# Performance work log

Hardware: AMD Instinct MI355X
Metric: run time of the kernel (lower is better)

## Reference

```python
import jax, jax.numpy as jnp
import numpy as np

N_NODES = 50000
N_EDGES = 600000
D_FEAT = 128
NHID = 128
N_CLASSES = 40


def gcn_conv(x, W, b, src, dst, n_nodes):
    """PyG-style GCNConv: out = D^{-1/2} (A + I) D^{-1/2} (x W) + b.

    src/dst: [E'] edge endpoints including self-loops; messages are gathered
    from src and scatter-added at dst with symmetric normalization.
    """
    h = x @ W  # [N, out] -- transform before propagate (linearity => same math)
    deg = jax.ops.segment_sum(jnp.ones_like(dst, dtype=h.dtype), dst,
                              num_segments=n_nodes)  # in-degree incl. self-loop
    dinv = jnp.where(deg > 0, jax.lax.rsqrt(deg), 0.0)
    norm = dinv[src] * dinv[dst]  # [E']
    msg = h[src] * norm[:, None]  # [E', out] gather + scale
    out = jax.ops.segment_sum(msg, dst, num_segments=n_nodes)  # scatter-add
    return out + b


def setup_inputs() -> dict:
    key = jax.random.key(0)
    ks = jax.random.split(key, 8)
    x = jax.random.normal(ks[0], (N_NODES, D_FEAT), dtype=jnp.float32)
    edge_index = jax.random.randint(ks[1], (2, N_EDGES), 0, N_NODES, dtype=jnp.int64)
    # Glorot-ish scaled params
    W1 = jax.random.normal(ks[2], (D_FEAT, NHID), dtype=jnp.float32) / np.sqrt(D_FEAT)
    b1 = jnp.zeros((NHID,), dtype=jnp.float32)
    W2 = jax.random.normal(ks[3], (NHID, NHID), dtype=jnp.float32) / np.sqrt(NHID)
    b2 = jnp.zeros((NHID,), dtype=jnp.float32)
    Wlin = jax.random.normal(ks[4], (NHID, N_CLASSES), dtype=jnp.float32) / np.sqrt(NHID)
    blin = jnp.zeros((N_CLASSES,), dtype=jnp.float32)
    return {"x": x, "edge_index": edge_index, "W1": W1, "b1": b1,
            "W2": W2, "b2": b2, "Wlin": Wlin, "blin": blin}


def reference(x, edge_index, W1, b1, W2, b2, Wlin, blin):
    n = x.shape[0]
    loop = jnp.arange(n, dtype=edge_index.dtype)
    src = jnp.concatenate([edge_index[0], loop])  # add self-loops
    dst = jnp.concatenate([edge_index[1], loop])
    h = gcn_conv(x, W1, b1, src, dst, n)
    h = jnp.tanh(h)  # dropout is identity in eval mode
    h = gcn_conv(h, W2, b2, src, dst, n)
    h = jnp.tanh(h)
    return h @ Wlin + blin  # [N, num_classes]
```

## Files before the change

### kernel.cpp

```cpp
#include <hip/hip_runtime.h>
#include <cmath>

#define D 128
#define NCLS 40
#define GG 391
#define CAP 64

typedef __bf16 bfrag __attribute__((ext_vector_type(8)));
typedef float ffrag __attribute__((ext_vector_type(4)));
typedef unsigned int u32;
typedef unsigned int u32x4 __attribute__((ext_vector_type(4)));

__device__ inline float fast_tanh(float x) {
  float ax = __builtin_fabsf(x);
  float z = __expf(-2.0f * ax);
  float r = (1.0f - z) * __builtin_amdgcn_rcpf(1.0f + z);
  return copysignf(r, x);
}

__global__ __launch_bounds__(256) void zero_deg(int* __restrict__ deg, int N) {
  int i = blockIdx.x * 256 + threadIdx.x;
  if (i < N) deg[i] = 0;
}

__global__ __launch_bounds__(256) void mega1(const float* __restrict__ A, const float* __restrict__ W1,
                                             const float* __restrict__ W2, const float* __restrict__ Wl,
                                             __bf16* __restrict__ C, int N,
                                             const int* __restrict__ src, const int* __restrict__ dst, int E,
                                             int* __restrict__ deg, int* __restrict__ csr,
                                             __bf16* __restrict__ Wt2, __bf16* __restrict__ Wlt, int EB) {
  const int b = blockIdx.x;
  const int tid = threadIdx.x;
  if (b >= GG) {
    if (b < GG + EB) {
      int e = (b - GG) * 256 + tid;
      if (e < E) {
        int s = src[e], d = dst[e];
        int pos = atomicAdd(&deg[d], 1);
        if (pos < CAP) csr[d * CAP + pos] = s;
      }
    } else {
      int j = (b - GG - EB) * 256 + tid;
      if (j < 16384) {
        Wt2[j] = (__bf16)W2[(j & 127) * D + (j >> 7)];
      } else if (j < 16384 + 48 * D) {
        int q = j - 16384;
        int n = q >> 7, k = q & 127;
        Wlt[q] = (n < NCLS) ? (__bf16)Wl[k * NCLS + n] : (__bf16)0.0f;
      }
    }
    return;
  }
  __shared__ __align__(16) __bf16 Bs[128][136];
  const int wave = tid >> 6, lane = tid & 63;
  const int row0 = b * 128 + wave * 32;
  const int koff = (lane >> 4) * 8;

  for (int i = tid; i < 128 * 128; i += 256) {
    int n = i & 127, k = i >> 7;
    Bs[n][k] = (__bf16)W1[k * D + n];
  }

  bfrag a[2][4];
#pragma unroll
  for (int mt = 0; mt < 2; ++mt) {
    int r = row0 + mt * 16 + (lane & 15);
    int rc = r < N ? r : N - 1;
    const float* p = A + (size_t)rc * D;
#pragma unroll
    for (int kk = 0; kk < 4; ++kk) {
      float4 u = *(const float4*)(p + kk * 32 + koff);
      float4 v = *(const float4*)(p + kk * 32 + koff + 4);
      bfrag f;
      f[0] = (__bf16)u.x; f[1] = (__bf16)u.y; f[2] = (__bf16)u.z; f[3] = (__bf16)u.w;
      f[4] = (__bf16)v.x; f[5] = (__bf16)v.y; f[6] = (__bf16)v.z; f[7] = (__bf16)v.w;
      a[mt][kk] = f;
    }
  }
  __syncthreads();

  ffrag acc[2][8];
#pragma unroll
  for (int mt = 0; mt < 2; ++mt)
#pragma unroll
    for (int n = 0; n < 8; ++n) acc[mt][n] = (ffrag){0.f, 0.f, 0.f, 0.f};

#pragma unroll
  for (int kk = 0; kk < 4; ++kk) {
#pragma unroll
    for (int n = 0; n < 8; ++n) {
      bfrag bb = *(const bfrag*)(&Bs[n * 16 + (lane & 15)][kk * 32 + koff]);
      acc[0][n] = __builtin_amdgcn_mfma_f32_16x16x32_bf16(a[0][kk], bb, acc[0][n], 0, 0, 0);
      acc[1][n] = __builtin_amdgcn_mfma_f32_16x16x32_bf16(a[1][kk], bb, acc[1][n], 0, 0, 0);
    }
  }

  int ocol = lane & 15;
#pragma unroll
  for (int mt = 0; mt < 2; ++mt) {
    int orow0 = row0 + mt * 16 + (lane >> 4) * 4;
#pragma unroll
    for (int n = 0; n < 8; ++n)
#pragma unroll
      for (int i = 0; i < 4; ++i) {
        int r = orow0 + i;
        if (r < N) C[(size_t)r * D + n * 16 + ocol] = (__bf16)acc[mt][n][i];
      }
  }
}

__device__ inline void gather16(const __bf16* __restrict__ t, const int* __restrict__ deg,
                                const int* __restrict__ csr, const float* __restrict__ bias,
                                __bf16 (*Hs)[136], int node0, int wave, int lane, int N) {
  const int g = lane >> 4, sl = lane & 15;
  const int nbase = node0 + wave * 4;

  int nd0 = nbase < N ? nbase : N - 1;
  int cnt0 = __builtin_amdgcn_readfirstlane(deg[nd0]);
  int jm0 = cnt0 < CAP ? cnt0 : CAP;
  int es0 = (lane < jm0) ? csr[nd0 * CAP + lane] : 0;
  int dg0 = deg[es0];
  bfrag tv0 = *(const bfrag*)(t + (size_t)nd0 * D + sl * 8);

#pragma unroll
  for (int m = 0; m < 4; ++m) {
    int cnt1 = 0, jm1 = 0, es1 = 0, dg1 = 0;
    bfrag tv1 = tv0;
    if (m < 3) {
      int nx = nbase + m + 1;
      int nd1 = nx < N ? nx : N - 1;
      cnt1 = __builtin_amdgcn_readfirstlane(deg[nd1]);
      jm1 = cnt1 < CAP ? cnt1 : CAP;
      es1 = (lane < jm1) ? csr[nd1 * CAP + lane] : 0;
      dg1 = deg[es1];
      tv1 = *(const bfrag*)(t + (size_t)nd1 * D + sl * 8);
    }

    float dv = rsqrtf((float)cnt0 + 1.0f);
    float ew = rsqrtf((float)dg0 + 1.0f) * dv;
    float selfw = (g == 0) ? dv * dv : 0.0f;
    float acc[8];
#pragma unroll
    for (int i = 0; i < 8; ++i) acc[i] = selfw * (float)tv0[i];

    for (int j = 0; j < jm0; j += 4) {
      int idx = j + g;
      int c = idx < jm0 ? idx : jm0 - 1;
      int s = __shfl(es0, c, 64);
      float wv = __shfl(ew, c, 64);
      float w = idx < jm0 ? wv : 0.0f;
      bfrag r = *(const bfrag*)(t + (size_t)s * D + sl * 8);
#pragma unroll
      for (int i = 0; i < 8; ++i) acc[i] += w * (float)r[i];
    }
#pragma unroll
    for (int i = 0; i < 8; ++i) {
      acc[i] += __shfl_xor(acc[i], 16, 64);
      acc[i] += __shfl_xor(acc[i], 32, 64);
    }

    if (g == 0) {
      float4 b0 = *(const float4*)(bias + sl * 8);
      float4 b1 = *(const float4*)(bias + sl * 8 + 4);
      bfrag o;
      o[0] = (__bf16)fast_tanh(acc[0] + b0.x);
      o[1] = (__bf16)fast_tanh(acc[1] + b0.y);
      o[2] = (__bf16)fast_tanh(acc[2] + b0.z);
      o[3] = (__bf16)fast_tanh(acc[3] + b0.w);
      o[4] = (__bf16)fast_tanh(acc[4] + b1.x);
      o[5] = (__bf16)fast_tanh(acc[5] + b1.y);
      o[6] = (__bf16)fast_tanh(acc[6] + b1.z);
      o[7] = (__bf16)fast_tanh(acc[7] + b1.w);
      *(u32x4*)&Hs[wave * 4 + m][sl * 8] = *(u32x4*)&o;
    }

    cnt0 = cnt1; jm0 = jm1; es0 = es1; dg0 = dg1; tv0 = tv1;
  }
}

__global__ __launch_bounds__(256) void gather_gemm(const __bf16* __restrict__ t, const int* __restrict__ deg,
                                                   const int* __restrict__ csr, const float* __restrict__ bias,
                                                   const __bf16* __restrict__ Wt, __bf16* __restrict__ C, int N) {
  __shared__ __align__(16) __bf16 Hs[16][136];
  const int tid = threadIdx.x;
  const int wave = tid >> 6, lane = tid & 63;
  const int g = lane >> 4, sl = lane & 15;
  const int node0 = blockIdx.x * 16;

  gather16(t, deg, csr, bias, Hs, node0, wave, lane, N);
  __syncthreads();

  const int koff = g * 8;
  bfrag a[4];
#pragma unroll
  for (int kk = 0; kk < 4; ++kk) a[kk] = *(const bfrag*)(&Hs[sl][kk * 32 + koff]);
  ffrag acc2[2];
  acc2[0] = (ffrag){0.f, 0.f, 0.f, 0.f};
  acc2[1] = (ffrag){0.f, 0.f, 0.f, 0.f};
#pragma unroll
  for (int nt = 0; nt < 2; ++nt) {
    const __bf16* wp = Wt + (size_t)(wave * 32 + nt * 16 + sl) * D;
    bfrag bfr[4];
#pragma unroll
    for (int kk = 0; kk < 4; ++kk) bfr[kk] = *(const bfrag*)(wp + kk * 32 + koff);
#pragma unroll
    for (int kk = 0; kk < 4; ++kk)
      acc2[nt] = __builtin_amdgcn_mfma_f32_16x16x32_bf16(a[kk], bfr[kk], acc2[nt], 0, 0, 0);
  }
#pragma unroll
  for (int nt = 0; nt < 2; ++nt) {
    int ccol = wave * 32 + nt * 16 + sl;
#pragma unroll
    for (int i = 0; i < 4; ++i) {
      int r = node0 + g * 4 + i;
      if (r < N) C[(size_t)r * D + ccol] = (__bf16)acc2[nt][i];
    }
  }
}

__global__ __launch_bounds__(256) void gather_head(const __bf16* __restrict__ t, const int* __restrict__ deg,
                                                   const int* __restrict__ csr, const float* __restrict__ bias,
                                                   const __bf16* __restrict__ Wlt, const float* __restrict__ blin,
                                                   float* __restrict__ out, int N) {
  __shared__ __align__(16) __bf16 Hs[16][136];
  const int tid = threadIdx.x;
  const int wave = tid >> 6, lane = tid & 63;
  const int g = lane >> 4, sl = lane & 15;
  const int node0 = blockIdx.x * 16;

  gather16(t, deg, csr, bias, Hs, node0, wave, lane, N);
  __syncthreads();

  if (wave < 3) {
    const int koff = g * 8;
    bfrag a[4];
#pragma unroll
    for (int kk = 0; kk < 4; ++kk) a[kk] = *(const bfrag*)(&Hs[sl][kk * 32 + koff]);
    ffrag acc2 = (ffrag){0.f, 0.f, 0.f, 0.f};
    const __bf16* wp = Wlt + (size_t)(wave * 16 + sl) * D;
    bfrag bfr[4];
#pragma unroll
    for (int kk = 0; kk < 4; ++kk) bfr[kk] = *(const bfrag*)(wp + kk * 32 + koff);
#pragma unroll
    for (int kk = 0; kk < 4; ++kk)
      acc2 = __builtin_amdgcn_mfma_f32_16x16x32_bf16(a[kk], bfr[kk], acc2, 0, 0, 0);

    int ccol = wave * 16 + sl;
    if (ccol < NCLS) {
      float bl = blin[ccol];
#pragma unroll
      for (int i = 0; i < 4; ++i) {
        int r = node0 + g * 4 + i;
        if (r < N) out[(size_t)r * NCLS + ccol] = acc2[i] + bl;
      }
    }
  }
}

extern "C" void kernel_launch(void* const* d_in, const int* in_sizes, int n_in,
                              void* d_out, int out_size, void* d_ws, size_t ws_size,
                              hipStream_t stream) {
  const float* x    = (const float*)d_in[0];
  const int*   ei   = (const int*)d_in[1];
  const float* W1   = (const float*)d_in[2];
  const float* b1   = (const float*)d_in[3];
  const float* W2   = (const float*)d_in[4];
  const float* b2   = (const float*)d_in[5];
  const float* Wlin = (const float*)d_in[6];
  const float* blin = (const float*)d_in[7];
  float* out = (float*)d_out;

  const int N = in_sizes[0] / D;
  const int E = in_sizes[1] / 2;
  const int* srcp = ei;
  const int* dstp = ei + E;

  char* ws = (char*)d_ws;
  int*    deg = (int*)ws;
  __bf16* Wt2 = (__bf16*)(ws + ((size_t)256 << 10));
  __bf16* Wlt = (__bf16*)(ws + ((size_t)320 << 10));
  int*    csr = (int*)(ws + ((size_t)1 << 20));
  __bf16* tb  = (__bf16*)(ws + ((size_t)16 << 20));
  __bf16* hb  = (__bf16*)(ws + ((size_t)32 << 20));

  const int nb = (N + 255) / 256;
  const int eb = (E + 255) / 256;
  const int cvb = (16384 + 48 * D + 255) / 256;
  const int gb = (N + 15) / 16;
  dim3 b256(256);

  zero_deg<<<nb, b256, 0, stream>>>(deg, N);
  mega1<<<GG + eb + cvb, b256, 0, stream>>>(x, W1, W2, Wlin, tb, N, srcp, dstp, E, deg, csr, Wt2, Wlt, eb);
  gather_gemm<<<gb, b256, 0, stream>>>(tb, deg, csr, b1, Wt2, hb, N);
  gather_head<<<gb, b256, 0, stream>>>(hb, deg, csr, b2, Wlt, blin, out, N);
}
```

Baseline: 203.4 us.

## Map one node per 16-lane group in gather instead of serial nodes per wave

The gather phase now assigns each of the four 16-lane groups in a wave its own destination node, instead of processing four nodes one after another with the neighbours split across groups. This removes the cross-group shuffle reduction and the serial per-node loop, and the four nodes' gathers proceed in parallel. Each group walks its neighbours in chunks of 16 loaded cooperatively. The wave's loop bound is now the maximum degree among its four nodes, and groups with fewer neighbours still step through the extra iterations, loading and multiplying with zero weights. The software prefetch of the next node's metadata is dropped.

```diff
diff --git a/kernel.cpp b/kernel.cpp
--- a/kernel.cpp
+++ b/kernel.cpp
@@ -113,69 +113,55 @@
                                 const int* __restrict__ csr, const float* __restrict__ bias,
                                 __bf16 (*Hs)[136], int node0, int wave, int lane, int N) {
   const int g = lane >> 4, sl = lane & 15;
-  const int nbase = node0 + wave * 4;
-
-  int nd0 = nbase < N ? nbase : N - 1;
-  int cnt0 = __builtin_amdgcn_readfirstlane(deg[nd0]);
-  int jm0 = cnt0 < CAP ? cnt0 : CAP;
-  int es0 = (lane < jm0) ? csr[nd0 * CAP + lane] : 0;
-  int dg0 = deg[es0];
-  bfrag tv0 = *(const bfrag*)(t + (size_t)nd0 * D + sl * 8);
-
-#pragma unroll
-  for (int m = 0; m < 4; ++m) {
-    int cnt1 = 0, jm1 = 0, es1 = 0, dg1 = 0;
-    bfrag tv1 = tv0;
-    if (m < 3) {
-      int nx = nbase + m + 1;
-      int nd1 = nx < N ? nx : N - 1;
-      cnt1 = __builtin_amdgcn_readfirstlane(deg[nd1]);
-      jm1 = cnt1 < CAP ? cnt1 : CAP;
-      es1 = (lane < jm1) ? csr[nd1 * CAP + lane] : 0;
-      dg1 = deg[es1];
-      tv1 = *(const bfrag*)(t + (size_t)nd1 * D + sl * 8);
-    }
-
-    float dv = rsqrtf((float)cnt0 + 1.0f);
-    float ew = rsqrtf((float)dg0 + 1.0f) * dv;
-    float selfw = (g == 0) ? dv * dv : 0.0f;
-    float acc[8];
-#pragma unroll
-    for (int i = 0; i < 8; ++i) acc[i] = selfw * (float)tv0[i];
-
-    for (int j = 0; j < jm0; j += 4) {
-      int idx = j + g;
-      int c = idx < jm0 ? idx : jm0 - 1;
-      int s = __shfl(es0, c, 64);
-      float wv = __shfl(ew, c, 64);
-      float w = idx < jm0 ? wv : 0.0f;
+  const int node = node0 + wave * 4 + g;
+  const int nd = node < N ? node : N - 1;
+  const int cnt = deg[nd];
+  const int jm = cnt < CAP ? cnt : CAP;
+  const float dv = rsqrtf((float)cnt + 1.0f);
+
+  int mx = jm;
+  int o1 = __shfl_xor(mx, 16, 64);
+  mx = mx > o1 ? mx : o1;
+  int o2 = __shfl_xor(mx, 32, 64);
+  mx = mx > o2 ? mx : o2;
+  const int jmw = __builtin_amdgcn_readfirstlane(mx);
+
+  bfrag tv = *(const bfrag*)(t + (size_t)nd * D + sl * 8);
+  const float selfw = dv * dv;
+  float acc[8];
+#pragma unroll
+  for (int i = 0; i < 8; ++i) acc[i] = selfw * (float)tv[i];
+
+  for (int base = 0; base < jmw; base += 16) {
+    int rem = jm - base;
+    int es = nd;
+    float ew = 0.0f;
+    if (sl < rem) {
+      es = csr[nd * CAP + base + sl];
+      ew = rsqrtf((float)deg[es] + 1.0f) * dv;
+    }
+    int nin = jmw - base; nin = nin < 16 ? nin : 16;
+    for (int j = 0; j < nin; ++j) {
+      int s = __shfl(es, g * 16 + j, 64);
+      float w = __shfl(ew, g * 16 + j, 64);
       bfrag r = *(const bfrag*)(t + (size_t)s * D + sl * 8);
 #pragma unroll
       for (int i = 0; i < 8; ++i) acc[i] += w * (float)r[i];
     }
-#pragma unroll
-    for (int i = 0; i < 8; ++i) {
-      acc[i] += __shfl_xor(acc[i], 16, 64);
-      acc[i] += __shfl_xor(acc[i], 32, 64);
-    }
-
-    if (g == 0) {
-      float4 b0 = *(const float4*)(bias + sl * 8);
-      float4 b1 = *(const float4*)(bias + sl * 8 + 4);
-      bfrag o;
-      o[0] = (__bf16)fast_tanh(acc[0] + b0.x);
-      o[1] = (__bf16)fast_tanh(acc[1] + b0.y);
-      o[2] = (__bf16)fast_tanh(acc[2] + b0.z);
-      o[3] = (__bf16)fast_tanh(acc[3] + b0.w);
-      o[4] = (__bf16)fast_tanh(acc[4] + b1.x);
-      o[5] = (__bf16)fast_tanh(acc[5] + b1.y);
-      o[6] = (__bf16)fast_tanh(acc[6] + b1.z);
-      o[7] = (__bf16)fast_tanh(acc[7] + b1.w);
-      *(u32x4*)&Hs[wave * 4 + m][sl * 8] = *(u32x4*)&o;
-    }
-
-    cnt0 = cnt1; jm0 = jm1; es0 = es1; dg0 = dg1; tv0 = tv1;
-  }
+  }
+
+  float4 b0 = *(const float4*)(bias + sl * 8);
+  float4 b1 = *(const float4*)(bias + sl * 8 + 4);
+  bfrag o;
+  o[0] = (__bf16)fast_tanh(acc[0] + b0.x);
+  o[1] = (__bf16)fast_tanh(acc[1] + b0.y);
+  o[2] = (__bf16)fast_tanh(acc[2] + b0.z);
+  o[3] = (__bf16)fast_tanh(acc[3] + b0.w);
+  o[4] = (__bf16)fast_tanh(acc[4] + b1.x);
+  o[5] = (__bf16)fast_tanh(acc[5] + b1.y);
+  o[6] = (__bf16)fast_tanh(acc[6] + b1.z);
+  o[7] = (__bf16)fast_tanh(acc[7] + b1.w);
+  *(u32x4*)&Hs[wave * 4 + g][sl * 8] = *(u32x4*)&o;
 }
 
 __global__ __launch_bounds__(256) void gather_gemm(const __bf16* __restrict__ t, const int* __restrict__ deg,
```

Result: faster. 188.4 us (-7.4%).
